# Optimization experiments

Measured on AMD Instinct MI355X. Metric: run time of the kernel, lower is better.

Reference implementation:

```python
import jax, jax.numpy as jnp
import numpy as np

B, N, C, D = 64, 1024, 128, 64

def setup_inputs() -> dict:
    key = jax.random.key(0)
    ks = jax.random.split(key, 7)
    # kaiming_normal_ on weights (fan_in = C), default zero-ish biases kept as Linear default uniform; use small uniform
    std = float(np.sqrt(2.0 / C))
    bb = float(1.0 / np.sqrt(C))
    return {
        "x": jax.random.normal(ks[0], (B, N, C), jnp.float32),
        "Wq": jax.random.normal(ks[1], (C, D), jnp.float32) * std,
        "bq": jax.random.uniform(ks[2], (D,), jnp.float32, -bb, bb),
        "Wk": jax.random.normal(ks[3], (C, D), jnp.float32) * std,
        "bk": jax.random.uniform(ks[4], (D,), jnp.float32, -bb, bb),
        "Wv": jax.random.normal(ks[5], (C, D), jnp.float32) * std,
        "bv": jax.random.uniform(ks[6], (D,), jnp.float32, -bb, bb),
    }

def reference(x, Wq, bq, Wk, bk, Wv, bv):
    q = jax.nn.relu(jnp.einsum('bnc,cd->bnd', x, Wq) + bq)  # [B,N,D]
    k = jax.nn.relu(jnp.einsum('bnc,cd->bnd', x, Wk) + bk)
    v = jax.nn.relu(jnp.einsum('bnc,cd->bnd', x, Wv) + bv)
    scores = jnp.einsum('bnd,bmd->bnm', q, k) / jnp.sqrt(jnp.asarray(D, q.dtype))
    attn = jax.nn.softmax(scores, axis=-1)
    out = jnp.einsum('bnm,bmd->bnd', attn, v)
    return out + q
```

## Files before the change

### kernel.cpp

```cpp
#include <hip/hip_runtime.h>
#include <hip/hip_bf16.h>


#define Bsz 64
#define Nsz 1024
#define Csz 128
#define Dsz 64

typedef __attribute__((ext_vector_type(8))) short short8;
typedef __attribute__((ext_vector_type(4))) float f32x4;

__device__ __forceinline__ unsigned short f2bf(float f) {
    union { float f; unsigned u; } v; v.f = f;
    unsigned r = v.u + 0x7FFF + ((v.u >> 16) & 1);
    return (unsigned short)(r >> 16);
}
__device__ __forceinline__ float bf2f(unsigned short h) {
    union { unsigned u; float f; } v; v.u = ((unsigned)h) << 16;
    return v.f;
}
__device__ __forceinline__ unsigned pack_bf16rn(float lo, float hi) {
    unsigned ulo = __float_as_uint(lo) + 0x8000u;
    unsigned uhi = __float_as_uint(hi) + 0x8000u;
    return __builtin_amdgcn_perm(uhi, ulo, 0x07060302u);
}

#define SCq (0.125f * 1.44269504f)
#define INV_SC (1.0f / (0.125f * 1.44269504f))

__global__ __launch_bounds__(256) void wprep_kernel(
    const float* __restrict__ Wq, const float* __restrict__ Wk,
    const float* __restrict__ Wv, unsigned short* __restrict__ wfrag)
{
    int t = blockIdx.x * 256 + threadIdx.x;
    int lane = t & 63, ksi = (t >> 6) & 3, dt = t >> 8;
    int l16 = lane & 15, quad = lane >> 4;
    int d = dt * 16 + l16;
    int c0 = ksi * 32 + quad * 8;
    short8 h8, l8, k8, v8;
    #pragma unroll
    for (int j = 0; j < 8; j++) {
        float w = Wq[(c0 + j) * Dsz + d];
        unsigned short h = f2bf(w);
        h8[j] = (short)h;
        l8[j] = (short)f2bf(w - bf2f(h));
        k8[j] = (short)f2bf(Wk[(c0 + j) * Dsz + d]);
        v8[j] = (short)f2bf(Wv[(c0 + j) * Dsz + d]);
    }
    int idx = (dt * 4 + ksi) * 64 + lane;
    ((short8*)wfrag)[0 * 1024 + idx] = h8;
    ((short8*)wfrag)[1 * 1024 + idx] = l8;
    ((short8*)wfrag)[2 * 1024 + idx] = k8;
    ((short8*)wfrag)[3 * 1024 + idx] = v8;
}

__global__ __launch_bounds__(256) void qkv_kernel(
    const float* __restrict__ x, const unsigned short* __restrict__ wfrag,
    const float* __restrict__ bq, const float* __restrict__ bk,
    const float* __restrict__ bv,
    unsigned short* __restrict__ qs, unsigned short* __restrict__ ks2,
    unsigned short* __restrict__ vt2)
{
    __shared__ short xh[8192];
    __shared__ short xl[8192];
    const int t    = threadIdx.x;
    const int lane = t & 63;
    const int l16  = lane & 15, quad = lane >> 4;
    const int dt   = t >> 6;
    const long rowbase = (long)blockIdx.x * 64;
    const int d = dt * 16 + l16;

    short8 wqh[4], wql[4], wkf[4], wvf[4];
    #pragma unroll
    for (int ksi = 0; ksi < 4; ksi++) {
        int idx = (dt * 4 + ksi) * 64 + lane;
        wqh[ksi] = ((const short8*)wfrag)[0 * 1024 + idx];
        wql[ksi] = ((const short8*)wfrag)[1 * 1024 + idx];
        wkf[ksi] = ((const short8*)wfrag)[2 * 1024 + idx];
        wvf[ksi] = ((const short8*)wfrag)[3 * 1024 + idx];
    }

    {
        const int row = t & 63;
        const float* xrow = x + (rowbase + row) * Csz;
        #pragma unroll
        for (int p = 0; p < 4; p++) {
            int cb = (t >> 6) + p * 4;
            float4 a = *(const float4*)(xrow + cb * 8);
            float4 bb = *(const float4*)(xrow + cb * 8 + 4);
            float f[8] = {a.x, a.y, a.z, a.w, bb.x, bb.y, bb.z, bb.w};
            short8 hi, lo;
            #pragma unroll
            for (int i = 0; i < 8; i++) {
                unsigned short h = f2bf(f[i]);
                hi[i] = (short)h;
                lo[i] = (short)f2bf(f[i] - bf2f(h));
            }
            int unit = ((row >> 4) * 4 + (cb >> 2)) * 64 + ((row & 15) | ((cb & 3) << 4));
            *(short8*)&xh[unit * 8] = hi;
            *(short8*)&xl[unit * 8] = lo;
        }
    }
    __syncthreads();

    f32x4 aq[4], ak[4], av[4];
    #pragma unroll
    for (int i = 0; i < 4; i++) {
        aq[i] = (f32x4){0.f, 0.f, 0.f, 0.f};
        ak[i] = (f32x4){0.f, 0.f, 0.f, 0.f};
        av[i] = (f32x4){0.f, 0.f, 0.f, 0.f};
    }
    #pragma unroll
    for (int ksi = 0; ksi < 4; ksi++) {
        #pragma unroll
        for (int rt = 0; rt < 4; rt++) {
            short8 ah = *(const short8*)&xh[((rt * 4 + ksi) * 64 + lane) * 8];
            short8 al = *(const short8*)&xl[((rt * 4 + ksi) * 64 + lane) * 8];
            aq[rt] = __builtin_amdgcn_mfma_f32_16x16x32_bf16(ah, wqh[ksi], aq[rt], 0, 0, 0);
            aq[rt] = __builtin_amdgcn_mfma_f32_16x16x32_bf16(al, wqh[ksi], aq[rt], 0, 0, 0);
            aq[rt] = __builtin_amdgcn_mfma_f32_16x16x32_bf16(ah, wql[ksi], aq[rt], 0, 0, 0);
            ak[rt] = __builtin_amdgcn_mfma_f32_16x16x32_bf16(ah, wkf[ksi], ak[rt], 0, 0, 0);
            av[rt] = __builtin_amdgcn_mfma_f32_16x16x32_bf16(ah, wvf[ksi], av[rt], 0, 0, 0);
        }
    }

    const float bqd = bq[d], bkd = bk[d], bvd = bv[d];
    const long b  = rowbase >> 10;
    const int  kt = (int)((rowbase >> 6) & 15);

    const int half  = dt >> 1;
    const int quadk = ((dt & 1) << 1) | (l16 >> 3);
    const int jk    = l16 & 7;
    unsigned short* kbase = ks2 + ((((long)(b * 16 + kt) * 4) * 2 + half) * 64) * 8;

    float vv[4][4];
    #pragma unroll
    for (int rt = 0; rt < 4; rt++) {
        #pragma unroll
        for (int r = 0; r < 4; r++) {
            long n = rowbase + rt * 16 + quad * 4 + r;
            float q = fmaxf(aq[rt][r] + bqd, 0.f);
            float k = fmaxf(ak[rt][r] + bkd, 0.f);
            vv[r][rt] = fmaxf(av[rt][r] + bvd, 0.f);
            qs[n * Dsz + d] = f2bf(q * SCq);
            kbase[((long)rt * 2 * 64 + quadk * 16 + quad * 4 + r) * 8 + jk] = f2bf(k);
        }
    }
    const int ck = quad >> 1;
    const int quadp = (quad & 1) * 2;
    long vidx = (((long)(b * 16 + kt) * 4 + dt) * 2 + ck) * 64 + quadp * 16 + l16;
    uint4 o0 = make_uint4(pack_bf16rn(vv[0][0], vv[0][1]), pack_bf16rn(vv[0][2], vv[0][3]),
                          pack_bf16rn(vv[1][0], vv[1][1]), pack_bf16rn(vv[1][2], vv[1][3]));
    uint4 o1 = make_uint4(pack_bf16rn(vv[2][0], vv[2][1]), pack_bf16rn(vv[2][2], vv[2][3]),
                          pack_bf16rn(vv[3][0], vv[3][1]), pack_bf16rn(vv[3][2], vv[3][3]));
    ((uint4*)vt2)[vidx]      = o0;
    ((uint4*)vt2)[vidx + 16] = o1;
}

__global__ __launch_bounds__(256) void attn_kernel(
    const unsigned short* __restrict__ qs,
    const unsigned short* __restrict__ ks2,
    const unsigned short* __restrict__ vt2,
    float* __restrict__ out)
{
    __shared__ short Pl[4][32][72];

    const int t    = threadIdx.x;
    const int wave = t >> 6;
    const int lane = t & 63;
    const int l16  = lane & 15;
    const int quad = lane >> 4;
    const int b    = blockIdx.x & 63;
    const int qh   = blockIdx.x >> 6;
    const int qbase = qh * 128 + wave * 32;

    const short8* ks8 = (const short8*)ks2 + (long)b * (16 * 4 * 2 * 64);
    const short8* vt8 = (const short8*)vt2 + (long)b * (16 * 4 * 2 * 64);

    short8 aq[2][2];
    #pragma unroll
    for (int s = 0; s < 2; s++) {
        const unsigned short* qp = qs + ((long)b * Nsz + qbase + s * 16 + l16) * Dsz + quad * 8;
        aq[s][0] = *(const short8*)(qp);
        aq[s][1] = *(const short8*)(qp + 32);
    }

    f32x4 O[2][4];
    float lsum[2][4];
    #pragma unroll
    for (int s = 0; s < 2; s++)
        #pragma unroll
        for (int i = 0; i < 4; i++) { O[s][i] = (f32x4){0.f,0.f,0.f,0.f}; lsum[s][i] = 0.f; }

    short8 kf[4][2];
    #pragma unroll
    for (int kb = 0; kb < 4; kb++) {
        kf[kb][0] = ks8[(kb * 2 + 0) * 64 + lane];
        kf[kb][1] = ks8[(kb * 2 + 1) * 64 + lane];
    }

    for (int kt = 0; kt < 16; kt++) {
        short8 bvf[2][4];
        #pragma unroll
        for (int cb = 0; cb < 4; cb++) {
            bvf[0][cb] = vt8[((long)kt * 8 + cb * 2 + 0) * 64 + lane];
            bvf[1][cb] = vt8[((long)kt * 8 + cb * 2 + 1) * 64 + lane];
        }

        f32x4 sc[2][4];
        #pragma unroll
        for (int s = 0; s < 2; s++) {
            #pragma unroll
            for (int kb = 0; kb < 4; kb++) {
                f32x4 z = (f32x4){0.f, 0.f, 0.f, 0.f};
                z = __builtin_amdgcn_mfma_f32_16x16x32_bf16(aq[s][0], kf[kb][0], z, 0, 0, 0);
                z = __builtin_amdgcn_mfma_f32_16x16x32_bf16(aq[s][1], kf[kb][1], z, 0, 0, 0);
                sc[s][kb] = z;
            }
        }

        short8 kf2[4][2];
        {
            int ktn = (kt + 1) & 15;
            #pragma unroll
            for (int kb = 0; kb < 4; kb++) {
                kf2[kb][0] = ks8[((long)ktn * 8 + kb * 2 + 0) * 64 + lane];
                kf2[kb][1] = ks8[((long)ktn * 8 + kb * 2 + 1) * 64 + lane];
            }
        }

        #pragma unroll
        for (int s = 0; s < 2; s++) {
            #pragma unroll
            for (int r = 0; r < 4; r++) {
                float p0 = __builtin_amdgcn_exp2f(sc[s][0][r]);
                float p1 = __builtin_amdgcn_exp2f(sc[s][1][r]);
                float p2 = __builtin_amdgcn_exp2f(sc[s][2][r]);
                float p3 = __builtin_amdgcn_exp2f(sc[s][3][r]);
                lsum[s][r] += (p0 + p1) + (p2 + p3);
                *(uint2*)&Pl[wave][s * 16 + quad * 4 + r][l16 * 4] =
                    make_uint2(pack_bf16rn(p0, p1), pack_bf16rn(p2, p3));
            }
        }

        #pragma unroll
        for (int ck = 0; ck < 2; ck++) {
            #pragma unroll
            for (int s = 0; s < 2; s++) {
                short8 ap = *(const short8*)&Pl[wave][s * 16 + l16][ck * 32 + quad * 8];
                #pragma unroll
                for (int cb = 0; cb < 4; cb++) {
                    O[s][cb] = __builtin_amdgcn_mfma_f32_16x16x32_bf16(ap, bvf[ck][cb], O[s][cb], 0, 0, 0);
                }
            }
        }

        #pragma unroll
        for (int kb = 0; kb < 4; kb++) { kf[kb][0] = kf2[kb][0]; kf[kb][1] = kf2[kb][1]; }
    }

    #pragma unroll
    for (int s = 0; s < 2; s++)
        #pragma unroll
        for (int r = 0; r < 4; r++)
            #pragma unroll
            for (int off = 1; off < 16; off <<= 1)
                lsum[s][r] += __shfl_xor(lsum[s][r], off);

    #pragma unroll
    for (int s = 0; s < 2; s++) {
        #pragma unroll
        for (int r = 0; r < 4; r++) {
            float rl = 1.0f / lsum[s][r];
            long nrow = (long)b * Nsz + qbase + s * 16 + quad * 4 + r;
            #pragma unroll
            for (int cb = 0; cb < 4; cb++) {
                int d = cb * 16 + l16;
                float qv = bf2f(qs[nrow * Dsz + d]) * INV_SC;
                out[nrow * Dsz + d] = O[s][cb][r] * rl + qv;
            }
        }
    }
}

extern "C" void kernel_launch(void* const* d_in, const int* in_sizes, int n_in,
                              void* d_out, int out_size, void* d_ws, size_t ws_size,
                              hipStream_t stream) {
    const float* x  = (const float*)d_in[0];
    const float* Wq = (const float*)d_in[1];
    const float* bq = (const float*)d_in[2];
    const float* Wk = (const float*)d_in[3];
    const float* bk = (const float*)d_in[4];
    const float* Wv = (const float*)d_in[5];
    const float* bv = (const float*)d_in[6];
    float* out = (float*)d_out;

    char* ws = (char*)d_ws;
    unsigned short* qsc   = (unsigned short*)ws;
    unsigned short* ks2   = (unsigned short*)(ws + 0x1000000);
    unsigned short* vt2   = (unsigned short*)(ws + 0x2000000);
    unsigned short* wfrag = (unsigned short*)(ws + 0x3000000);

    wprep_kernel<<<dim3(4), dim3(256), 0, stream>>>(Wq, Wk, Wv, wfrag);
    qkv_kernel<<<dim3(1024), dim3(256), 0, stream>>>(
        x, wfrag, bq, bk, bv, qsc, ks2, vt2);
    attn_kernel<<<dim3(512), dim3(256), 0, stream>>>(
        qsc, ks2, vt2, out);
}
```

Before: 120.7 us.

## Interleave QK MFMA with exp per half-tile, remap qkv blocks, add occupancy bound

The attention loop is split into two 16-row halves. The exp/pack work for the first half now overlaps with the QK^T MFMAs of the second half, and the V fragment loads are staggered. The qkv kernel remaps block indices so that consecutive blocks cover different batches in a swizzled order, which may change L2 and channel locality. Attention launch bounds now request two blocks per CU, which may constrain registers and risk spills.

```diff
diff --git a/kernel.cpp b/kernel.cpp
--- a/kernel.cpp
+++ b/kernel.cpp
@@ -67,7 +67,12 @@
     const int lane = t & 63;
     const int l16  = lane & 15, quad = lane >> 4;
     const int dt   = t >> 6;
-    const long rowbase = (long)blockIdx.x * 64;
+    const int blk = blockIdx.x;
+    const int r8  = blk & 7;
+    const int m   = blk >> 3;
+    const int bat = r8 + 8 * (m >> 4);
+    const int til = m & 15;
+    const long rowbase = ((long)bat * 16 + til) * 64;
     const int d = dt * 16 + l16;
 
     short8 wqh[4], wql[4], wkf[4], wvf[4];
@@ -157,7 +162,7 @@
     ((uint4*)vt2)[vidx + 16] = o1;
 }
 
-__global__ __launch_bounds__(256) void attn_kernel(
+__global__ __launch_bounds__(256, 2) void attn_kernel(
     const unsigned short* __restrict__ qs,
     const unsigned short* __restrict__ ks2,
     const unsigned short* __restrict__ vt2,
@@ -200,23 +205,42 @@
     }
 
     for (int kt = 0; kt < 16; kt++) {
-        short8 bvf[2][4];
-        #pragma unroll
-        for (int cb = 0; cb < 4; cb++) {
-            bvf[0][cb] = vt8[((long)kt * 8 + cb * 2 + 0) * 64 + lane];
-            bvf[1][cb] = vt8[((long)kt * 8 + cb * 2 + 1) * 64 + lane];
-        }
-
-        f32x4 sc[2][4];
-        #pragma unroll
-        for (int s = 0; s < 2; s++) {
-            #pragma unroll
-            for (int kb = 0; kb < 4; kb++) {
-                f32x4 z = (f32x4){0.f, 0.f, 0.f, 0.f};
-                z = __builtin_amdgcn_mfma_f32_16x16x32_bf16(aq[s][0], kf[kb][0], z, 0, 0, 0);
-                z = __builtin_amdgcn_mfma_f32_16x16x32_bf16(aq[s][1], kf[kb][1], z, 0, 0, 0);
-                sc[s][kb] = z;
-            }
+        short8 bv0[4], bv1[4];
+        #pragma unroll
+        for (int cb = 0; cb < 4; cb++)
+            bv0[cb] = vt8[((long)kt * 8 + cb * 2 + 0) * 64 + lane];
+
+        f32x4 sc0[4];
+        #pragma unroll
+        for (int kb = 0; kb < 4; kb++) {
+            f32x4 z = (f32x4){0.f, 0.f, 0.f, 0.f};
+            z = __builtin_amdgcn_mfma_f32_16x16x32_bf16(aq[0][0], kf[kb][0], z, 0, 0, 0);
+            z = __builtin_amdgcn_mfma_f32_16x16x32_bf16(aq[0][1], kf[kb][1], z, 0, 0, 0);
+            sc0[kb] = z;
+        }
+
+        #pragma unroll
+        for (int cb = 0; cb < 4; cb++)
+            bv1[cb] = vt8[((long)kt * 8 + cb * 2 + 1) * 64 + lane];
+
+        #pragma unroll
+        for (int r = 0; r < 4; r++) {
+            float p0 = __builtin_amdgcn_exp2f(sc0[0][r]);
+            float p1 = __builtin_amdgcn_exp2f(sc0[1][r]);
+            float p2 = __builtin_amdgcn_exp2f(sc0[2][r]);
+            float p3 = __builtin_amdgcn_exp2f(sc0[3][r]);
+            lsum[0][r] += (p0 + p1) + (p2 + p3);
+            *(uint2*)&Pl[wave][quad * 4 + r][l16 * 4] =
+                make_uint2(pack_bf16rn(p0, p1), pack_bf16rn(p2, p3));
+        }
+
+        f32x4 sc1[4];
+        #pragma unroll
+        for (int kb = 0; kb < 4; kb++) {
+            f32x4 z = (f32x4){0.f, 0.f, 0.f, 0.f};
+            z = __builtin_amdgcn_mfma_f32_16x16x32_bf16(aq[1][0], kf[kb][0], z, 0, 0, 0);
+            z = __builtin_amdgcn_mfma_f32_16x16x32_bf16(aq[1][1], kf[kb][1], z, 0, 0, 0);
+            sc1[kb] = z;
         }
 
         short8 kf2[4][2];
@@ -230,29 +254,29 @@
         }
 
         #pragma unroll
+        for (int r = 0; r < 4; r++) {
+            float p0 = __builtin_amdgcn_exp2f(sc1[0][r]);
+            float p1 = __builtin_amdgcn_exp2f(sc1[1][r]);
+            float p2 = __builtin_amdgcn_exp2f(sc1[2][r]);
+            float p3 = __builtin_amdgcn_exp2f(sc1[3][r]);
+            lsum[1][r] += (p0 + p1) + (p2 + p3);
+            *(uint2*)&Pl[wave][16 + quad * 4 + r][l16 * 4] =
+                make_uint2(pack_bf16rn(p0, p1), pack_bf16rn(p2, p3));
+        }
+
+        #pragma unroll
         for (int s = 0; s < 2; s++) {
-            #pragma unroll
-            for (int r = 0; r < 4; r++) {
-                float p0 = __builtin_amdgcn_exp2f(sc[s][0][r]);
-                float p1 = __builtin_amdgcn_exp2f(sc[s][1][r]);
-                float p2 = __builtin_amdgcn_exp2f(sc[s][2][r]);
-                float p3 = __builtin_amdgcn_exp2f(sc[s][3][r]);
-                lsum[s][r] += (p0 + p1) + (p2 + p3);
-                *(uint2*)&Pl[wave][s * 16 + quad * 4 + r][l16 * 4] =
-                    make_uint2(pack_bf16rn(p0, p1), pack_bf16rn(p2, p3));
-            }
-        }
-
-        #pragma unroll
-        for (int ck = 0; ck < 2; ck++) {
-            #pragma unroll
-            for (int s = 0; s < 2; s++) {
-                short8 ap = *(const short8*)&Pl[wave][s * 16 + l16][ck * 32 + quad * 8];
-                #pragma unroll
-                for (int cb = 0; cb < 4; cb++) {
-                    O[s][cb] = __builtin_amdgcn_mfma_f32_16x16x32_bf16(ap, bvf[ck][cb], O[s][cb], 0, 0, 0);
-                }
-            }
+            short8 ap = *(const short8*)&Pl[wave][s * 16 + l16][quad * 8];
+            #pragma unroll
+            for (int cb = 0; cb < 4; cb++)
+                O[s][cb] = __builtin_amdgcn_mfma_f32_16x16x32_bf16(ap, bv0[cb], O[s][cb], 0, 0, 0);
+        }
+        #pragma unroll
+        for (int s = 0; s < 2; s++) {
+            short8 ap = *(const short8*)&Pl[wave][s * 16 + l16][32 + quad * 8];
+            #pragma unroll
+            for (int cb = 0; cb < 4; cb++)
+                O[s][cb] = __builtin_amdgcn_mfma_f32_16x16x32_bf16(ap, bv1[cb], O[s][cb], 0, 0, 0);
         }
 
         #pragma unroll
```

Measured after the change: 128.8 us. 6.7% more time.
